# Optimization experiments

Measured on AMD Instinct MI355X. Metric: run time of the kernel, lower is better.

Reference implementation:

```python
import jax, jax.numpy as jnp
import numpy as np

N = 100000
E = 1600000
IN_DIM = 128
HID = 64
TDIM = 16
OUT_DIM = 2
NEG_SLOPE = 0.01  # F.leaky_relu default


def _linear_params(key, fan_in, fan_out):
    kw, kb = jax.random.split(key)
    s = 1.0 / np.sqrt(fan_in)
    w = jax.random.uniform(kw, (fan_in, fan_out), jnp.float32, -s, s)
    b = jax.random.uniform(kb, (fan_out,), jnp.float32, -s, s)
    return w, b


def setup_inputs() -> dict:
    key = jax.random.key(0)
    ks = jax.random.split(key, 12)
    x = jax.random.normal(ks[0], (N, IN_DIM), jnp.float32)
    edge_index = jax.random.randint(ks[1], (2, E), 0, N, jnp.int32)
    edge_time = jax.random.uniform(ks[2], (E, 1), jnp.float32)

    lin1_w, lin1_b = _linear_params(ks[3], IN_DIM, HID)
    attn1_w, attn1_b = _linear_params(ks[4], 2 * HID + TDIM, 1)
    t1_w, t1_b = _linear_params(ks[5], 1, TDIM)

    lin2_w, lin2_b = _linear_params(ks[6], HID, HID)
    attn2_w, attn2_b = _linear_params(ks[7], 2 * HID + TDIM, 1)
    t2_w, t2_b = _linear_params(ks[8], 1, TDIM)

    cls_w, cls_b = _linear_params(ks[9], HID, OUT_DIM)

    return dict(x=x, edge_index=edge_index, edge_time=edge_time,
                lin1_w=lin1_w, lin1_b=lin1_b, attn1_w=attn1_w, attn1_b=attn1_b,
                t1_w=t1_w, t1_b=t1_b,
                lin2_w=lin2_w, lin2_b=lin2_b, attn2_w=attn2_w, attn2_b=attn2_b,
                t2_w=t2_w, t2_b=t2_b, cls_w=cls_w, cls_b=cls_b)


def _segment_softmax(a, index, num_segments):
    # PyG softmax over variable-size neighborhoods grouped by destination node
    m = jax.ops.segment_max(a, index, num_segments=num_segments)
    e = jnp.exp(a - m[index])
    s = jax.ops.segment_sum(e, index, num_segments=num_segments)
    return e / (s[index] + 1e-16)


def _temporal_gat_conv(x, src, dst, edge_time,
                       lin_w, lin_b, attn_w, attn_b, t_w, t_b):
    # TemporalEncoding: sin(Linear(1, time_dim)(t))  -> [E, TDIM]
    t_enc = jnp.sin(edge_time @ t_w + t_b)
    # lin applied per-edge to x_i and x_j == lin applied once at node level then gathered
    h = x @ lin_w + lin_b                      # [N, HID]
    h_i = h[dst]                               # [E, HID] target features
    h_j = h[src]                               # [E, HID] source features
    alpha_in = jnp.concatenate([h_i, h_j, t_enc], axis=1)   # [E, 2*HID+TDIM]
    alpha = jax.nn.leaky_relu(alpha_in @ attn_w + attn_b, NEG_SLOPE)  # [E, 1]
    alpha = _segment_softmax(alpha, dst, x.shape[0])
    msg = h_j * alpha                          # [E, HID]
    return jax.ops.segment_sum(msg, dst, num_segments=x.shape[0])  # aggr='add'


def reference(x, edge_index, edge_time,
              lin1_w, lin1_b, attn1_w, attn1_b, t1_w, t1_b,
              lin2_w, lin2_b, attn2_w, attn2_b, t2_w, t2_b,
              cls_w, cls_b):
    src = edge_index[0]  # j (source)
    dst = edge_index[1]  # i (target / softmax segment index)
    h = _temporal_gat_conv(x, src, dst, edge_time,
                           lin1_w, lin1_b, attn1_w, attn1_b, t1_w, t1_b)
    h = jax.nn.relu(h)
    # dropout p=0.3 is identity in eval mode
    h = _temporal_gat_conv(h, src, dst, edge_time,
                           lin2_w, lin2_b, attn2_w, attn2_b, t2_w, t2_b)
    return h @ cls_w + cls_b  # [N, OUT_DIM]
```

## Files before the change

### kernel.cpp

```cpp
#include <hip/hip_runtime.h>

typedef unsigned short u16;
typedef unsigned int u32;

typedef __attribute__((ext_vector_type(8))) short short8v;
typedef __attribute__((ext_vector_type(4))) float float4v;

__device__ __forceinline__ float bf2f(u16 u) {
    return __uint_as_float(((u32)u) << 16);
}
__device__ __forceinline__ u16 f2bf(float f) {
    u32 u = __float_as_uint(f);
    u32 r = (u + 0x7fffu + ((u >> 16) & 1u)) >> 16;
    return (u16)r;
}
__device__ __forceinline__ float ldf(const void* p, int i, int isf32) {
    return isf32 ? ((const float*)p)[i] : bf2f(((const u16*)p)[i]);
}

#define P_W1   0
#define P_W2   8192
#define P_B1   12288
#define P_B2   12352
#define P_A1W  12416
#define P_A1B  12560
#define P_T1W  12561
#define P_T1B  12577
#define P_A2W  12593
#define P_A2B  12737
#define P_T2W  12738
#define P_T2B  12754
#define P_CLSW 12770
#define P_CLSB 12898
#define P_TOT  12900

#define CH   4096
#define NCHB 256
#define CAP  128

#define W1F_ELEMS 16384
#define W2F_ELEMS 8192

__global__ __launch_bounds__(256) void detect_dtype(
    const u32* __restrict__ xw, int nwords, int* __restrict__ flag)
{
    __shared__ int sbad;
    if (threadIdx.x == 0) sbad = 0;
    __syncthreads();
    int bad = 0;
    for (int i = threadIdx.x; i < nwords; i += 256) {
        u32 w = xw[i];
        int ea = (w >> 7) & 0xff;
        if (ea >= 0xF0) bad = 1;
    }
    if (bad) sbad = 1;
    __syncthreads();
    if (threadIdx.x == 0) flag[0] = sbad;
}

__global__ __launch_bounds__(256) void prep_params(
    const void* l1w, const void* l1b, const void* a1w, const void* a1b,
    const void* t1w, const void* t1b, const void* l2w, const void* l2b,
    const void* a2w, const void* a2b, const void* t2w, const void* t2b,
    const void* clsw, const void* clsb,
    const int* __restrict__ flag, float* __restrict__ P,
    u16* __restrict__ w1h, u16* __restrict__ w1l,
    u16* __restrict__ w2h, u16* __restrict__ w2l)
{
    const int f = flag[0];
    const int t = blockIdx.x * 256 + threadIdx.x;
    const int stride = gridDim.x * 256;
#define SEG(src, off, cnt) for (int i = t; i < (cnt); i += stride) P[(off) + i] = ldf(src, i, f)
    SEG(l1w, P_W1, 8192);
    SEG(l2w, P_W2, 4096);
    SEG(l1b, P_B1, 64);
    SEG(l2b, P_B2, 64);
    SEG(a1w, P_A1W, 144);
    SEG(a1b, P_A1B, 1);
    SEG(t1w, P_T1W, 16);
    SEG(t1b, P_T1B, 16);
    SEG(a2w, P_A2W, 144);
    SEG(a2b, P_A2B, 1);
    SEG(t2w, P_T2W, 16);
    SEG(t2b, P_T2B, 16);
    SEG(clsw, P_CLSW, 128);
    SEG(clsb, P_CLSB, 2);
#undef SEG
    for (int e = t; e < W1F_ELEMS + W2F_ELEMS; e += stride) {
        int idx;
        const void* wsrc;
        u16 *dh, *dl;
        if (e < W1F_ELEMS) { idx = e; wsrc = l1w; dh = w1h; dl = w1l; }
        else { idx = e - W1F_ELEMS; wsrc = l2w; dh = w2h; dl = w2l; }
        int j = idx & 7;
        int l = (idx >> 3) & 63;
        int ctks = idx >> 9;
        int ct = ctks & 3;
        int ks = ctks >> 2;
        int k = ks * 32 + (l >> 4) * 8 + j;
        int col = ct * 16 + (l & 15);
        float wv = ldf(wsrc, k * 64 + col, f);
        u16 hh = f2bf(wv);
        dh[idx] = hh;
        dl[idx] = f2bf(wv - bf2f(hh));
    }
}

template<int K, int XMODE>
__global__ __launch_bounds__(256) void node_gemm_mfma(
    const void* __restrict__ xin, const float* __restrict__ P,
    int BOFF, int AOFF, const int* __restrict__ flag,
    const u16* __restrict__ wfh, const u16* __restrict__ wfl,
    u32* __restrict__ houtb, float* __restrict__ si, float* __restrict__ sj,
    int nnodes)
{
    const int l = threadIdx.x & 63;
    const int w = threadIdx.x >> 6;
    const int cl = l & 15;
    const int cg = l >> 4;
    const int rowbase = blockIdx.x * 64 + w * 16;
    const bool xf32 = (XMODE == 0) ? (flag[0] != 0) : false;

    const int arow = rowbase + cl;
    const int arc = (arow < nnodes) ? arow : 0;
    const int kb = cg * 8;

    const u16* xb = (const u16*)xin;
    const float* xf = (const float*)xin;
    const short8v* bhp = (const short8v*)wfh;
    const short8v* blp = (const short8v*)wfl;

    float4v acc[4];
    #pragma unroll
    for (int ct = 0; ct < 4; ++ct) acc[ct] = (float4v){0.f, 0.f, 0.f, 0.f};

    #pragma unroll
    for (int ks = 0; ks < K / 32; ++ks) {
        short8v ah, al_;
        bool hasl = false;
        if (XMODE == 2 || !xf32) {
            ah = *(const short8v*)&xb[(size_t)arc * K + ks * 32 + kb];
            al_ = (short8v){0, 0, 0, 0, 0, 0, 0, 0};
        } else {
            float4 v0 = *(const float4*)&xf[(size_t)arc * K + ks * 32 + kb];
            float4 v1 = *(const float4*)&xf[(size_t)arc * K + ks * 32 + kb + 4];
            float fv[8] = { v0.x, v0.y, v0.z, v0.w, v1.x, v1.y, v1.z, v1.w };
            #pragma unroll
            for (int j = 0; j < 8; ++j) {
                u32 u = __float_as_uint(fv[j]);
                ah[j] = (short)(u >> 16);
                float hif = __uint_as_float(u & 0xffff0000u);
                al_[j] = (short)f2bf(fv[j] - hif);
            }
            hasl = true;
        }
        #pragma unroll
        for (int ct = 0; ct < 4; ++ct) {
            short8v bh = bhp[(ks * 4 + ct) * 64 + l];
            short8v bl = blp[(ks * 4 + ct) * 64 + l];
            acc[ct] = __builtin_amdgcn_mfma_f32_16x16x32_bf16(ah, bh, acc[ct], 0, 0, 0);
            acc[ct] = __builtin_amdgcn_mfma_f32_16x16x32_bf16(ah, bl, acc[ct], 0, 0, 0);
            if (hasl)
                acc[ct] = __builtin_amdgcn_mfma_f32_16x16x32_bf16(al_, bh, acc[ct], 0, 0, 0);
        }
    }

    #pragma unroll
    for (int r = 0; r < 4; ++r) {
        int node = rowbase + cg * 4 + r;
        float aiv = 0.f, ajv = 0.f;
        u16 hs[4];
        #pragma unroll
        for (int ct = 0; ct < 4; ++ct) {
            float v = acc[ct][r] + P[BOFF + ct * 16 + cl];
            aiv = fmaf(v, P[AOFF + ct * 16 + cl], aiv);
            ajv = fmaf(v, P[AOFF + 64 + ct * 16 + cl], ajv);
            hs[ct] = f2bf(v);
        }
        #pragma unroll
        for (int o = 1; o < 16; o <<= 1) {
            aiv += __shfl_xor(aiv, o);
            ajv += __shfl_xor(ajv, o);
        }
        if (node < nnodes) {
            u16* hp = (u16*)houtb + (size_t)node * 64 + cl;
            hp[0] = hs[0]; hp[16] = hs[1]; hp[32] = hs[2]; hp[48] = hs[3];
            if (cl == 0) { si[node] = aiv; sj[node] = ajv; }
        }
    }
}

__global__ __launch_bounds__(256) void count_chunks(
    const int* __restrict__ eid, int* __restrict__ chunkhist, int E)
{
    __shared__ int hist[NCHB];
    const int t = threadIdx.x, c = blockIdx.x;
    hist[t] = 0;
    __syncthreads();
    const int base = c * CH;
    #pragma unroll
    for (int i = 0; i < CH / 256; ++i) {
        int e = base + t + i * 256;
        if (e < E) atomicAdd(&hist[eid[e] >> 9], 1);
    }
    __syncthreads();
    chunkhist[c * NCHB + t] = hist[t];
}

__global__ __launch_bounds__(256) void scan_chunks(
    int* __restrict__ chunkhist, int* __restrict__ buckettot, int nchunks)
{
    __shared__ int s[512];
    const int b = blockIdx.x, t = threadIdx.x;
    int v0 = (t < nchunks) ? chunkhist[(size_t)t * NCHB + b] : 0;
    int v1 = (t + 256 < nchunks) ? chunkhist[(size_t)(t + 256) * NCHB + b] : 0;
    s[t] = v0; s[t + 256] = v1;
    __syncthreads();
    for (int off = 1; off < 512; off <<= 1) {
        int x0 = (t >= off) ? s[t - off] : 0;
        int x1 = s[t + 256 - off];
        __syncthreads();
        s[t] += x0; s[t + 256] += x1;
        __syncthreads();
    }
    if (t < nchunks) chunkhist[(size_t)t * NCHB + b] = s[t] - v0;
    if (t + 256 < nchunks) chunkhist[(size_t)(t + 256) * NCHB + b] = s[t + 256] - v1;
    if (t == 255) buckettot[b] = s[511];
}

__global__ __launch_bounds__(256) void bucket_start_scan(
    const int* __restrict__ buckettot, int* __restrict__ bucketstart,
    int* __restrict__ offs, int N)
{
    __shared__ int s[NCHB];
    const int b = threadIdx.x;
    int v = buckettot[b];
    s[b] = v;
    __syncthreads();
    for (int off = 1; off < NCHB; off <<= 1) {
        int x = (b >= off) ? s[b - off] : 0;
        __syncthreads();
        s[b] += x;
        __syncthreads();
    }
    bucketstart[b] = s[b] - v;
    if (b == NCHB - 1) { bucketstart[NCHB] = s[b]; offs[N] = s[b]; }
}

__global__ __launch_bounds__(256) void place_chunks(
    const int* __restrict__ ei, const void* __restrict__ et,
    const int* __restrict__ flag, const int* __restrict__ chunkhist,
    const int* __restrict__ bucketstart, int2* __restrict__ staging, int E)
{
    __shared__ int2 sorted[CH];
    __shared__ unsigned char bno[CH];
    __shared__ int hist[NCHB], lstart[NCHB], cur[NCHB], gb[NCHB];
    const int t = threadIdx.x, c = blockIdx.x;
    const int base = c * CH;
    const int f = flag[0];
    hist[t] = 0;
    gb[t] = bucketstart[t] + chunkhist[c * NCHB + t];
    __syncthreads();
    #pragma unroll
    for (int i = 0; i < CH / 256; ++i) {
        int e = base + t + i * 256;
        if (e < E) atomicAdd(&hist[ei[E + e] >> 9], 1);
    }
    __syncthreads();
    int v = hist[t];
    lstart[t] = v;
    __syncthreads();
    for (int off = 1; off < NCHB; off <<= 1) {
        int x = (t >= off) ? lstart[t - off] : 0;
        __syncthreads();
        lstart[t] += x;
        __syncthreads();
    }
    int ex = lstart[t] - v;
    __syncthreads();
    lstart[t] = ex;
    cur[t] = ex;
    __syncthreads();
    #pragma unroll
    for (int i = 0; i < CH / 256; ++i) {
        int e = base + t + i * 256;
        if (e < E) {
            int s_ = ei[e], d = ei[E + e];
            float tt = ldf(et, e, f);
            int b = d >> 9;
            int p = atomicAdd(&cur[b], 1);
            sorted[p] = make_int2(s_ | ((d & 511) << 17), __float_as_int(tt));
            bno[p] = (unsigned char)b;
        }
    }
    __syncthreads();
    const int cnt_tot = min(CH, E - base);
    for (int idx = t; idx < cnt_tot; idx += 256) {
        int b = bno[idx];
        staging[gb[b] + (idx - lstart[b])] = sorted[idx];
    }
}

__global__ __launch_bounds__(256) void bin_edges(
    const int2* __restrict__ staging, const int* __restrict__ bucketstart,
    int* __restrict__ offs, int2* __restrict__ csrA, int N)
{
    __shared__ int cnt[512], loc[512];
    const int b = blockIdx.x, t = threadIdx.x;
    const int beg = bucketstart[b], end = bucketstart[b + 1];
    const int nstart = b << 9;
    cnt[t] = 0; cnt[t + 256] = 0;
    __syncthreads();
    for (int i = beg + t; i < end; i += 256)
        atomicAdd(&cnt[(((u32)staging[i].x) >> 17) & 511], 1);
    __syncthreads();
    int v0 = cnt[t], v1 = cnt[t + 256];
    loc[t] = v0; loc[t + 256] = v1;
    __syncthreads();
    for (int off = 1; off < 512; off <<= 1) {
        int x0 = (t >= off) ? loc[t - off] : 0;
        int x1 = loc[t + 256 - off];
        __syncthreads();
        loc[t] += x0; loc[t + 256] += x1;
        __syncthreads();
    }
    int cur0 = beg + loc[t] - v0;
    int cur1 = beg + loc[t + 256] - v1;
    if (nstart + t < N) offs[nstart + t] = cur0;
    if (nstart + t + 256 < N) offs[nstart + t + 256] = cur1;
    cnt[t] = cur0; cnt[t + 256] = cur1;
    __syncthreads();
    for (int i = beg + t; i < end; i += 256) {
        int2 e = staging[i];
        int slot = atomicAdd(&cnt[(((u32)e.x) >> 17) & 511], 1);
        csrA[slot] = make_int2(e.x & 0x1ffff, e.y);
    }
}

template<int MODE>
__global__ __launch_bounds__(256) void aggregate(
    const int* __restrict__ offs, const int2* __restrict__ csr2,
    const u32* __restrict__ hb,
    const float* __restrict__ si, const float* __restrict__ sjv,
    const float* __restrict__ P,
    u32* __restrict__ houtb, void* __restrict__ outp,
    const int* __restrict__ flag, int n)
{
    constexpr int TW = (MODE == 0) ? P_T1W : P_T2W;
    constexpr int TB = (MODE == 0) ? P_T1B : P_T2B;
    constexpr int AW = (MODE == 0) ? P_A1W : P_A2W;
    constexpr int AB = (MODE == 0) ? P_A1B : P_A2B;

    __shared__ int2 cache[4][2][CAP];
    const int wave = threadIdx.x >> 6;
    const int lane = threadIdx.x & 63;
    const int half = lane >> 5;
    const int hl = lane & 31;
    const int node = blockIdx.x * 8 + wave * 2 + half;
    const bool active = node < n;
    int beg = 0, end = 0;
    if (active) { beg = offs[node]; end = offs[node + 1]; }
    const int deg = end - beg;
    int2* cw = cache[wave][half];
    const float sii = active ? si[node] : 0.f;

    float ssum = 0.f;
    for (int idx = hl; idx < deg; idx += 32) {
        int2 st = csr2[beg + idx];
        float tt = __int_as_float(st.y);
        float td = P[AB];
        #pragma unroll
        for (int k = 0; k < 16; ++k)
            td += __sinf(fmaf(tt, P[TW + k], P[TB + k])) * P[AW + 128 + k];
        float a = sii + sjv[st.x] + td;
        a = (a > 0.f) ? a : 0.01f * a;
        float e = __expf(fminf(a, 80.f));
        if (idx < CAP) cw[idx] = make_int2(st.x, __float_as_int(e));
        ssum += e;
    }
    #pragma unroll
    for (int o = 16; o > 0; o >>= 1) ssum += __shfl_xor(ssum, o);

    const int degc = min(deg, CAP);
    const int degpad = (degc + 7) & ~7;
    if (hl < degpad - degc) cw[degc + hl] = make_int2(0, 0);

    float ax = 0.f, ay = 0.f;
    for (int j0 = 0; j0 < degpad; j0 += 8) {
        int2 sv[8];
        u32 pv[8];
        #pragma unroll
        for (int q = 0; q < 8; ++q) sv[q] = cw[j0 + q];
        #pragma unroll
        for (int q = 0; q < 8; ++q) pv[q] = hb[sv[q].x * 32 + hl];
        #pragma unroll
        for (int q = 0; q < 8; ++q) {
            float e = __int_as_float(sv[q].y);
            ax = fmaf(e, __uint_as_float(pv[q] << 16), ax);
            ay = fmaf(e, __uint_as_float(pv[q] & 0xffff0000u), ay);
        }
    }
    for (int j = CAP; j < deg; ++j) {
        int2 st = csr2[beg + j];
        float tt = __int_as_float(st.y);
        float td = P[AB];
        #pragma unroll
        for (int k = 0; k < 16; ++k)
            td += __sinf(fmaf(tt, P[TW + k], P[TB + k])) * P[AW + 128 + k];
        float a = sii + sjv[st.x] + td;
        a = (a > 0.f) ? a : 0.01f * a;
        float e = __expf(fminf(a, 80.f));
        u32 pk = hb[st.x * 32 + hl];
        ax = fmaf(e, __uint_as_float(pk << 16), ax);
        ay = fmaf(e, __uint_as_float(pk & 0xffff0000u), ay);
    }

    if (!active) return;
    float inv = 1.0f / (ssum + 1e-16f);

    if (MODE == 0) {
        float r0 = fmaxf(ax * inv, 0.f);
        float r1 = fmaxf(ay * inv, 0.f);
        houtb[node * 32 + hl] = (u32)f2bf(r0) | ((u32)f2bf(r1) << 16);
    } else {
        float r0 = ax * inv, r1 = ay * inv;
        float l0 = r0 * P[P_CLSW + 4 * hl]     + r1 * P[P_CLSW + 4 * hl + 2];
        float l1 = r0 * P[P_CLSW + 4 * hl + 1] + r1 * P[P_CLSW + 4 * hl + 3];
        #pragma unroll
        for (int o = 16; o > 0; o >>= 1) {
            l0 += __shfl_xor(l0, o);
            l1 += __shfl_xor(l1, o);
        }
        if (hl == 0) {
            l0 += P[P_CLSB];
            l1 += P[P_CLSB + 1];
            if (flag[0]) {
                ((float2*)outp)[node] = make_float2(l0, l1);
            } else {
                ((u32*)outp)[node] = (u32)f2bf(l0) | ((u32)f2bf(l1) << 16);
            }
        }
    }
}

extern "C" void kernel_launch(void* const* d_in, const int* in_sizes, int n_in,
                              void* d_out, int out_size, void* d_ws, size_t ws_size,
                              hipStream_t stream)
{
    const void* x    = d_in[0];
    const int*  ei   = (const int*)d_in[1];
    const void* et   = d_in[2];
    const void* l1w  = d_in[3];
    const void* l1b  = d_in[4];
    const void* a1w  = d_in[5];
    const void* a1b  = d_in[6];
    const void* t1w  = d_in[7];
    const void* t1b  = d_in[8];
    const void* l2w  = d_in[9];
    const void* l2b  = d_in[10];
    const void* a2w  = d_in[11];
    const void* a2b  = d_in[12];
    const void* t2w  = d_in[13];
    const void* t2b  = d_in[14];
    const void* clsw = d_in[15];
    const void* clsb = d_in[16];

    const int N = in_sizes[0] / 128;
    const int E = in_sizes[2];
    const int nchunks = (E + CH - 1) / CH;
    const int nbkt = (N + 511) >> 9;

    char* ws = (char*)d_ws;
    size_t off = 0;
    auto A = [&](size_t bytes) -> char* {
        char* p = ws + off;
        off = (off + bytes + 255) & ~(size_t)255;
        return p;
    };
    int*   flag        = (int*)A(256);
    float* P           = (float*)A(P_TOT * 4);
    u16*   w1fh        = (u16*)A(W1F_ELEMS * 2);
    u16*   w1fl        = (u16*)A(W1F_ELEMS * 2);
    u16*   w2fh        = (u16*)A(W2F_ELEMS * 2);
    u16*   w2fl        = (u16*)A(W2F_ELEMS * 2);
    u32*   h1b         = (u32*)A((size_t)N * 32 * 4);
    float* si1         = (float*)A((size_t)N * 4);
    float* sj1         = (float*)A((size_t)N * 4);
    float* si2         = (float*)A((size_t)N * 4);
    float* sj2         = (float*)A((size_t)N * 4);
    int*   chunkhist   = (int*)A((size_t)nchunks * NCHB * 4);
    int*   buckettot   = (int*)A(NCHB * 4);
    int*   bucketstart = (int*)A((size_t)(NCHB + 1) * 4);
    int*   offs        = (int*)A((size_t)(N + 1) * 4);
    int2*  csrA        = (int2*)A((size_t)E * 8);
    char*  unionr      = A((size_t)E * 8 < (size_t)N * 32 * 4
                           ? (size_t)N * 32 * 4 : (size_t)E * 8);
    int2*  staging     = (int2*)unionr;
    u32*   hagb        = (u32*)unionr;
    (void)ws_size; (void)n_in; (void)out_size;

    detect_dtype<<<1, 256, 0, stream>>>((const u32*)x, 4096, flag);

    prep_params<<<32, 256, 0, stream>>>(l1w, l1b, a1w, a1b, t1w, t1b,
                                        l2w, l2b, a2w, a2b, t2w, t2b,
                                        clsw, clsb, flag, P,
                                        w1fh, w1fl, w2fh, w2fl);

    node_gemm_mfma<128, 0><<<(N + 63) / 64, 256, 0, stream>>>(
        x, P, P_B1, P_A1W, flag, w1fh, w1fl, h1b, si1, sj1, N);

    count_chunks<<<nchunks, 256, 0, stream>>>(ei + E, chunkhist, E);

    scan_chunks<<<NCHB, 256, 0, stream>>>(chunkhist, buckettot, nchunks);

    bucket_start_scan<<<1, 256, 0, stream>>>(buckettot, bucketstart, offs, N);

    place_chunks<<<nchunks, 256, 0, stream>>>(ei, et, flag, chunkhist,
                                              bucketstart, staging, E);

    bin_edges<<<nbkt, 256, 0, stream>>>(staging, bucketstart, offs, csrA, N);

    aggregate<0><<<(N + 7) / 8, 256, 0, stream>>>(
        offs, csrA, h1b, si1, sj1, P, hagb, nullptr, flag, N);

    node_gemm_mfma<64, 2><<<(N + 63) / 64, 256, 0, stream>>>(
        hagb, P, P_B2, P_A2W, flag, w2fh, w2fl, h1b, si2, sj2, N);

    aggregate<1><<<(N + 7) / 8, 256, 0, stream>>>(
        offs, csrA, h1b, si2, sj2, P, nullptr, d_out, flag, N);
}
```

Before: 272.7 us.

## Merge setup kernels and assign 16 lanes per node in aggregation

Dtype detection, parameter prep and chunk counting now run as one launch. The chunk scan shares a launch with the first node GEMM, and the bucket-start scan is recomputed redundantly inside place_chunks and bin_edges, so the dependent chain has fewer launches. The aggregation kernel now gives each destination node a quarter wave (16 lanes) with 8-byte gathers of four bf16 features, where it previously used a half wave with 4-byte gathers. This is meant to cut launch and serialization overhead and waste on low-degree nodes, at the cost of redundant scans and fewer lanes per edge loop.

```diff
diff --git a/kernel.cpp b/kernel.cpp
--- a/kernel.cpp
+++ b/kernel.cpp
@@ -41,35 +41,51 @@
 #define W1F_ELEMS 16384
 #define W2F_ELEMS 8192
 
-__global__ __launch_bounds__(256) void detect_dtype(
-    const u32* __restrict__ xw, int nwords, int* __restrict__ flag)
-{
-    __shared__ int sbad;
-    if (threadIdx.x == 0) sbad = 0;
-    __syncthreads();
-    int bad = 0;
-    for (int i = threadIdx.x; i < nwords; i += 256) {
-        u32 w = xw[i];
-        int ea = (w >> 7) & 0xff;
-        if (ea >= 0xF0) bad = 1;
-    }
-    if (bad) sbad = 1;
-    __syncthreads();
-    if (threadIdx.x == 0) flag[0] = sbad;
-}
-
-__global__ __launch_bounds__(256) void prep_params(
+__global__ __launch_bounds__(256) void prep_and_count(
+    const u32* __restrict__ xw,
     const void* l1w, const void* l1b, const void* a1w, const void* a1b,
     const void* t1w, const void* t1b, const void* l2w, const void* l2b,
     const void* a2w, const void* a2b, const void* t2w, const void* t2b,
     const void* clsw, const void* clsb,
-    const int* __restrict__ flag, float* __restrict__ P,
+    int* __restrict__ flag, float* __restrict__ P,
     u16* __restrict__ w1h, u16* __restrict__ w1l,
-    u16* __restrict__ w2h, u16* __restrict__ w2l)
-{
-    const int f = flag[0];
-    const int t = blockIdx.x * 256 + threadIdx.x;
-    const int stride = gridDim.x * 256;
+    u16* __restrict__ w2h, u16* __restrict__ w2l,
+    const int* __restrict__ eid, int* __restrict__ chunkhist,
+    int E, int nchunks)
+{
+    if ((int)blockIdx.x < nchunks) {
+        __shared__ int hist[NCHB];
+        const int t = threadIdx.x, c = blockIdx.x;
+        hist[t] = 0;
+        __syncthreads();
+        const int base = c * CH;
+        #pragma unroll
+        for (int i = 0; i < CH / 256; ++i) {
+            int e = base + t + i * 256;
+            if (e < E) atomicAdd(&hist[eid[e] >> 9], 1);
+        }
+        __syncthreads();
+        chunkhist[c * NCHB + t] = hist[t];
+        return;
+    }
+
+    const int bid = blockIdx.x - nchunks;
+    __shared__ int sbad;
+    if (threadIdx.x == 0) sbad = 0;
+    __syncthreads();
+    int bad = 0;
+    for (int i = threadIdx.x; i < 4096; i += 256) {
+        u32 w = xw[i];
+        int ea = (w >> 7) & 0xff;
+        if (ea >= 0xF0) bad = 1;
+    }
+    if (bad) sbad = 1;
+    __syncthreads();
+    const int f = sbad;
+    if (bid == 0 && threadIdx.x == 0) flag[0] = f;
+
+    const int t = bid * 256 + threadIdx.x;
+    const int stride = 32 * 256;
 #define SEG(src, off, cnt) for (int i = t; i < (cnt); i += stride) P[(off) + i] = ldf(src, i, f)
     SEG(l1w, P_W1, 8192);
     SEG(l2w, P_W2, 4096);
@@ -107,8 +123,8 @@
 }
 
 template<int K, int XMODE>
-__global__ __launch_bounds__(256) void node_gemm_mfma(
-    const void* __restrict__ xin, const float* __restrict__ P,
+__device__ __forceinline__ void gemm_body(
+    int bid, const void* __restrict__ xin, const float* __restrict__ P,
     int BOFF, int AOFF, const int* __restrict__ flag,
     const u16* __restrict__ wfh, const u16* __restrict__ wfl,
     u32* __restrict__ houtb, float* __restrict__ si, float* __restrict__ sj,
@@ -118,7 +134,7 @@
     const int w = threadIdx.x >> 6;
     const int cl = l & 15;
     const int cg = l >> 4;
-    const int rowbase = blockIdx.x * 64 + w * 16;
+    const int rowbase = bid * 64 + w * 16;
     const bool xf32 = (XMODE == 0) ? (flag[0] != 0) : false;
 
     const int arow = rowbase + cl;
@@ -190,28 +206,12 @@
     }
 }
 
-__global__ __launch_bounds__(256) void count_chunks(
-    const int* __restrict__ eid, int* __restrict__ chunkhist, int E)
-{
-    __shared__ int hist[NCHB];
-    const int t = threadIdx.x, c = blockIdx.x;
-    hist[t] = 0;
-    __syncthreads();
-    const int base = c * CH;
-    #pragma unroll
-    for (int i = 0; i < CH / 256; ++i) {
-        int e = base + t + i * 256;
-        if (e < E) atomicAdd(&hist[eid[e] >> 9], 1);
-    }
-    __syncthreads();
-    chunkhist[c * NCHB + t] = hist[t];
-}
-
-__global__ __launch_bounds__(256) void scan_chunks(
-    int* __restrict__ chunkhist, int* __restrict__ buckettot, int nchunks)
+__device__ __forceinline__ void scan_body(
+    int b, int* __restrict__ chunkhist, int* __restrict__ buckettot,
+    int nchunks)
 {
     __shared__ int s[512];
-    const int b = blockIdx.x, t = threadIdx.x;
+    const int t = threadIdx.x;
     int v0 = (t < nchunks) ? chunkhist[(size_t)t * NCHB + b] : 0;
     int v1 = (t + 256 < nchunks) ? chunkhist[(size_t)(t + 256) * NCHB + b] : 0;
     s[t] = v0; s[t + 256] = v1;
@@ -228,39 +228,58 @@
     if (t == 255) buckettot[b] = s[511];
 }
 
-__global__ __launch_bounds__(256) void bucket_start_scan(
-    const int* __restrict__ buckettot, int* __restrict__ bucketstart,
-    int* __restrict__ offs, int N)
-{
-    __shared__ int s[NCHB];
-    const int b = threadIdx.x;
-    int v = buckettot[b];
-    s[b] = v;
-    __syncthreads();
-    for (int off = 1; off < NCHB; off <<= 1) {
-        int x = (b >= off) ? s[b - off] : 0;
-        __syncthreads();
-        s[b] += x;
-        __syncthreads();
-    }
-    bucketstart[b] = s[b] - v;
-    if (b == NCHB - 1) { bucketstart[NCHB] = s[b]; offs[N] = s[b]; }
+__global__ __launch_bounds__(256) void scan_and_gemm1(
+    int* __restrict__ chunkhist, int* __restrict__ buckettot, int nchunks,
+    const void* __restrict__ x, const float* __restrict__ P,
+    const int* __restrict__ flag,
+    const u16* __restrict__ w1h, const u16* __restrict__ w1l,
+    u32* __restrict__ h1b, float* __restrict__ si1, float* __restrict__ sj1,
+    int N)
+{
+    if (blockIdx.x < NCHB) {
+        scan_body(blockIdx.x, chunkhist, buckettot, nchunks);
+        return;
+    }
+    gemm_body<128, 0>(blockIdx.x - NCHB, x, P, P_B1, P_A1W, flag,
+                      w1h, w1l, h1b, si1, sj1, N);
+}
+
+__global__ __launch_bounds__(256) void node_gemm2(
+    const void* __restrict__ xin, const float* __restrict__ P,
+    const int* __restrict__ flag,
+    const u16* __restrict__ wfh, const u16* __restrict__ wfl,
+    u32* __restrict__ houtb, float* __restrict__ si, float* __restrict__ sj,
+    int nnodes)
+{
+    gemm_body<64, 2>(blockIdx.x, xin, P, P_B2, P_A2W, flag,
+                     wfh, wfl, houtb, si, sj, nnodes);
 }
 
 __global__ __launch_bounds__(256) void place_chunks(
     const int* __restrict__ ei, const void* __restrict__ et,
     const int* __restrict__ flag, const int* __restrict__ chunkhist,
-    const int* __restrict__ bucketstart, int2* __restrict__ staging, int E)
+    const int* __restrict__ buckettot, int2* __restrict__ staging, int E)
 {
     __shared__ int2 sorted[CH];
     __shared__ unsigned char bno[CH];
-    __shared__ int hist[NCHB], lstart[NCHB], cur[NCHB], gb[NCHB];
+    __shared__ int hist[NCHB], lstart[NCHB], cur[NCHB], gb[NCHB], bs[NCHB];
     const int t = threadIdx.x, c = blockIdx.x;
     const int base = c * CH;
     const int f = flag[0];
+
+    int bv = buckettot[t];
+    bs[t] = bv;
     hist[t] = 0;
-    gb[t] = bucketstart[t] + chunkhist[c * NCHB + t];
-    __syncthreads();
+    __syncthreads();
+    for (int off = 1; off < NCHB; off <<= 1) {
+        int x = (t >= off) ? bs[t - off] : 0;
+        __syncthreads();
+        bs[t] += x;
+        __syncthreads();
+    }
+    gb[t] = (bs[t] - bv) + chunkhist[c * NCHB + t];
+    __syncthreads();
+
     #pragma unroll
     for (int i = 0; i < CH / 256; ++i) {
         int e = base + t + i * 256;
@@ -302,15 +321,28 @@
 }
 
 __global__ __launch_bounds__(256) void bin_edges(
-    const int2* __restrict__ staging, const int* __restrict__ bucketstart,
-    int* __restrict__ offs, int2* __restrict__ csrA, int N)
-{
-    __shared__ int cnt[512], loc[512];
+    const int2* __restrict__ staging, const int* __restrict__ buckettot,
+    int* __restrict__ offs, int2* __restrict__ csrA, int N, int E)
+{
+    __shared__ int cnt[512], loc[512], bs[NCHB];
     const int b = blockIdx.x, t = threadIdx.x;
-    const int beg = bucketstart[b], end = bucketstart[b + 1];
+
+    int bv = buckettot[t];
+    bs[t] = bv;
+    cnt[t] = 0; cnt[t + 256] = 0;
+    __syncthreads();
+    for (int off = 1; off < NCHB; off <<= 1) {
+        int x = (t >= off) ? bs[t - off] : 0;
+        __syncthreads();
+        bs[t] += x;
+        __syncthreads();
+    }
+    const int end = bs[b];
+    const int beg = (b == 0) ? 0 : bs[b - 1];
+    if (b == 0 && t == 0) offs[N] = E;
     const int nstart = b << 9;
-    cnt[t] = 0; cnt[t + 256] = 0;
-    __syncthreads();
+    __syncthreads();
+
     for (int i = beg + t; i < end; i += 256)
         atomicAdd(&cnt[(((u32)staging[i].x) >> 17) & 511], 1);
     __syncthreads();
@@ -351,21 +383,21 @@
     constexpr int AW = (MODE == 0) ? P_A1W : P_A2W;
     constexpr int AB = (MODE == 0) ? P_A1B : P_A2B;
 
-    __shared__ int2 cache[4][2][CAP];
+    __shared__ int2 cache[4][4][CAP];
     const int wave = threadIdx.x >> 6;
     const int lane = threadIdx.x & 63;
-    const int half = lane >> 5;
-    const int hl = lane & 31;
-    const int node = blockIdx.x * 8 + wave * 2 + half;
+    const int q = lane >> 4;
+    const int ql = lane & 15;
+    const int node = blockIdx.x * 16 + wave * 4 + q;
     const bool active = node < n;
     int beg = 0, end = 0;
     if (active) { beg = offs[node]; end = offs[node + 1]; }
     const int deg = end - beg;
-    int2* cw = cache[wave][half];
+    int2* cw = cache[wave][q];
     const float sii = active ? si[node] : 0.f;
 
     float ssum = 0.f;
-    for (int idx = hl; idx < deg; idx += 32) {
+    for (int idx = ql; idx < deg; idx += 16) {
         int2 st = csr2[beg + idx];
         float tt = __int_as_float(st.y);
         float td = P[AB];
@@ -379,25 +411,28 @@
         ssum += e;
     }
     #pragma unroll
-    for (int o = 16; o > 0; o >>= 1) ssum += __shfl_xor(ssum, o);
+    for (int o = 8; o > 0; o >>= 1) ssum += __shfl_xor(ssum, o);
 
     const int degc = min(deg, CAP);
     const int degpad = (degc + 7) & ~7;
-    if (hl < degpad - degc) cw[degc + hl] = make_int2(0, 0);
-
-    float ax = 0.f, ay = 0.f;
+    if (ql < degpad - degc) cw[degc + ql] = make_int2(0, 0);
+
+    const uint2* hb2 = (const uint2*)hb;
+    float a0 = 0.f, a1 = 0.f, a2 = 0.f, a3 = 0.f;
     for (int j0 = 0; j0 < degpad; j0 += 8) {
         int2 sv[8];
-        u32 pv[8];
-        #pragma unroll
-        for (int q = 0; q < 8; ++q) sv[q] = cw[j0 + q];
-        #pragma unroll
-        for (int q = 0; q < 8; ++q) pv[q] = hb[sv[q].x * 32 + hl];
-        #pragma unroll
-        for (int q = 0; q < 8; ++q) {
-            float e = __int_as_float(sv[q].y);
-            ax = fmaf(e, __uint_as_float(pv[q] << 16), ax);
-            ay = fmaf(e, __uint_as_float(pv[q] & 0xffff0000u), ay);
+        uint2 pv[8];
+        #pragma unroll
+        for (int p = 0; p < 8; ++p) sv[p] = cw[j0 + p];
+        #pragma unroll
+        for (int p = 0; p < 8; ++p) pv[p] = hb2[sv[p].x * 16 + ql];
+        #pragma unroll
+        for (int p = 0; p < 8; ++p) {
+            float e = __int_as_float(sv[p].y);
+            a0 = fmaf(e, __uint_as_float(pv[p].x << 16), a0);
+            a1 = fmaf(e, __uint_as_float(pv[p].x & 0xffff0000u), a1);
+            a2 = fmaf(e, __uint_as_float(pv[p].y << 16), a2);
+            a3 = fmaf(e, __uint_as_float(pv[p].y & 0xffff0000u), a3);
         }
     }
     for (int j = CAP; j < deg; ++j) {
@@ -410,28 +445,37 @@
         float a = sii + sjv[st.x] + td;
         a = (a > 0.f) ? a : 0.01f * a;
         float e = __expf(fminf(a, 80.f));
-        u32 pk = hb[st.x * 32 + hl];
-        ax = fmaf(e, __uint_as_float(pk << 16), ax);
-        ay = fmaf(e, __uint_as_float(pk & 0xffff0000u), ay);
+        uint2 pk = hb2[st.x * 16 + ql];
+        a0 = fmaf(e, __uint_as_float(pk.x << 16), a0);
+        a1 = fmaf(e, __uint_as_float(pk.x & 0xffff0000u), a1);
+        a2 = fmaf(e, __uint_as_float(pk.y << 16), a2);
+        a3 = fmaf(e, __uint_as_float(pk.y & 0xffff0000u), a3);
     }
 
     if (!active) return;
     float inv = 1.0f / (ssum + 1e-16f);
 
     if (MODE == 0) {
-        float r0 = fmaxf(ax * inv, 0.f);
-        float r1 = fmaxf(ay * inv, 0.f);
-        houtb[node * 32 + hl] = (u32)f2bf(r0) | ((u32)f2bf(r1) << 16);
+        float r0 = fmaxf(a0 * inv, 0.f);
+        float r1 = fmaxf(a1 * inv, 0.f);
+        float r2 = fmaxf(a2 * inv, 0.f);
+        float r3 = fmaxf(a3 * inv, 0.f);
+        u32 w0 = (u32)f2bf(r0) | ((u32)f2bf(r1) << 16);
+        u32 w1 = (u32)f2bf(r2) | ((u32)f2bf(r3) << 16);
+        *(uint2*)&houtb[node * 32 + 2 * ql] = make_uint2(w0, w1);
     } else {
-        float r0 = ax * inv, r1 = ay * inv;
-        float l0 = r0 * P[P_CLSW + 4 * hl]     + r1 * P[P_CLSW + 4 * hl + 2];
-        float l1 = r0 * P[P_CLSW + 4 * hl + 1] + r1 * P[P_CLSW + 4 * hl + 3];
-        #pragma unroll
-        for (int o = 16; o > 0; o >>= 1) {
+        float r0 = a0 * inv, r1 = a1 * inv, r2 = a2 * inv, r3 = a3 * inv;
+        const int f0 = 4 * ql;
+        float l0 = r0 * P[P_CLSW + 2 * f0]     + r1 * P[P_CLSW + 2 * f0 + 2]
+                 + r2 * P[P_CLSW + 2 * f0 + 4] + r3 * P[P_CLSW + 2 * f0 + 6];
+        float l1 = r0 * P[P_CLSW + 2 * f0 + 1] + r1 * P[P_CLSW + 2 * f0 + 3]
+                 + r2 * P[P_CLSW + 2 * f0 + 5] + r3 * P[P_CLSW + 2 * f0 + 7];
+        #pragma unroll
+        for (int o = 8; o > 0; o >>= 1) {
             l0 += __shfl_xor(l0, o);
             l1 += __shfl_xor(l1, o);
         }
-        if (hl == 0) {
+        if (ql == 0) {
             l0 += P[P_CLSB];
             l1 += P[P_CLSB + 1];
             if (flag[0]) {
@@ -469,6 +513,7 @@
     const int E = in_sizes[2];
     const int nchunks = (E + CH - 1) / CH;
     const int nbkt = (N + 511) >> 9;
+    const int gblocks = (N + 63) / 64;
 
     char* ws = (char*)d_ws;
     size_t off = 0;
@@ -490,7 +535,6 @@
     float* sj2         = (float*)A((size_t)N * 4);
     int*   chunkhist   = (int*)A((size_t)nchunks * NCHB * 4);
     int*   buckettot   = (int*)A(NCHB * 4);
-    int*   bucketstart = (int*)A((size_t)(NCHB + 1) * 4);
     int*   offs        = (int*)A((size_t)(N + 1) * 4);
     int2*  csrA        = (int2*)A((size_t)E * 8);
     char*  unionr      = A((size_t)E * 8 < (size_t)N * 32 * 4
@@ -499,33 +543,27 @@
     u32*   hagb        = (u32*)unionr;
     (void)ws_size; (void)n_in; (void)out_size;
 
-    detect_dtype<<<1, 256, 0, stream>>>((const u32*)x, 4096, flag);
-
-    prep_params<<<32, 256, 0, stream>>>(l1w, l1b, a1w, a1b, t1w, t1b,
-                                        l2w, l2b, a2w, a2b, t2w, t2b,
-                                        clsw, clsb, flag, P,
-                                        w1fh, w1fl, w2fh, w2fl);
-
-    node_gemm_mfma<128, 0><<<(N + 63) / 64, 256, 0, stream>>>(
-        x, P, P_B1, P_A1W, flag, w1fh, w1fl, h1b, si1, sj1, N);
-
-    count_chunks<<<nchunks, 256, 0, stream>>>(ei + E, chunkhist, E);
-
-    scan_chunks<<<NCHB, 256, 0, stream>>>(chunkhist, buckettot, nchunks);
-
-    bucket_start_scan<<<1, 256, 0, stream>>>(buckettot, bucketstart, offs, N);
+    prep_and_count<<<nchunks + 32, 256, 0, stream>>>(
+        (const u32*)x, l1w, l1b, a1w, a1b, t1w, t1b,
+        l2w, l2b, a2w, a2b, t2w, t2b, clsw, clsb,
+        flag, P, w1fh, w1fl, w2fh, w2fl,
+        ei + E, chunkhist, E, nchunks);
+
+    scan_and_gemm1<<<NCHB + gblocks, 256, 0, stream>>>(
+        chunkhist, buckettot, nchunks,
+        x, P, flag, w1fh, w1fl, h1b, si1, sj1, N);
 
     place_chunks<<<nchunks, 256, 0, stream>>>(ei, et, flag, chunkhist,
-                                              bucketstart, staging, E);
-
-    bin_edges<<<nbkt, 256, 0, stream>>>(staging, bucketstart, offs, csrA, N);
-
-    aggregate<0><<<(N + 7) / 8, 256, 0, stream>>>(
+                                              buckettot, staging, E);
+
+    bin_edges<<<nbkt, 256, 0, stream>>>(staging, buckettot, offs, csrA, N, E);
+
+    aggregate<0><<<(N + 15) / 16, 256, 0, stream>>>(
         offs, csrA, h1b, si1, sj1, P, hagb, nullptr, flag, N);
 
-    node_gemm_mfma<64, 2><<<(N + 63) / 64, 256, 0, stream>>>(
-        hagb, P, P_B2, P_A2W, flag, w2fh, w2fl, h1b, si2, sj2, N);
-
-    aggregate<1><<<(N + 7) / 8, 256, 0, stream>>>(
+    node_gemm2<<<gblocks, 256, 0, stream>>>(
+        hagb, P, flag, w2fh, w2fl, h1b, si2, sj2, N);
+
+    aggregate<1><<<(N + 15) / 16, 256, 0, stream>>>(
         offs, csrA, h1b, si2, sj2, P, nullptr, d_out, flag, N);
 }
```

New measurement: 266.9 us. 1.02x faster.
